# Kernel optimization log

Hardware: AMD Instinct MI355X
Metric: run time of the kernel (lower is better)

## Reference

```python
import jax, jax.numpy as jnp
import numpy as np

B, N, D_IN, D_OUT, H = 4, 2048, 1024, 1024, 16
HEAD_DIM = D_OUT // H


def setup_inputs() -> dict:
    key = jax.random.key(0)
    k1, k2, k3 = jax.random.split(key, 3)
    x = jax.random.normal(k1, (B, N, D_IN), dtype=jnp.float32)
    # torch Linear: y = x @ W.T + b; we store W already transposed as [in, out]
    w_attn = jax.random.normal(k2, (D_IN, 3 * D_OUT), dtype=jnp.float32) * (1.0 / np.sqrt(D_IN))
    w_proj = jax.random.normal(k3, (D_OUT, D_OUT), dtype=jnp.float32) * (1.0 / np.sqrt(D_OUT))
    b_proj = jnp.zeros((D_OUT,), dtype=jnp.float32)
    return {"x": x, "w_attn": w_attn, "w_proj": w_proj, "b_proj": b_proj}


def reference(x, w_attn, w_proj, b_proj):
    b, n, _ = x.shape
    qkv = x @ w_attn  # [b, n, 3*d_out]
    q, k, v = jnp.split(qkv, 3, axis=2)
    # [b, n, d_out] -> [b, h, n, head_dim]
    def to_heads(t):
        return t.reshape(b, n, H, HEAD_DIM).transpose(0, 2, 1, 3)
    q, k, v = to_heads(q), to_heads(k), to_heads(v)
    scale = 1.0 / np.sqrt(HEAD_DIM).astype(np.float32)
    att = jnp.einsum('bhqd,bhkd->bhqk', q, k) * scale  # [b, h, n, n]
    causal = jnp.tril(jnp.ones((n, n), dtype=bool))  # True = keep
    att = jnp.where(causal, att, -jnp.inf)
    att = jax.nn.softmax(att, axis=-1)
    # dropout p=0.0 -> identity
    out = jnp.einsum('bhqk,bhkd->bhqd', att, v)  # [b, h, n, head_dim]
    out = out.transpose(0, 2, 1, 3).reshape(b, n, D_OUT)
    return out @ w_proj + b_proj
```

## Files before the change

### kernel.cpp

```cpp
#include <hip/hip_runtime.h>
#include <hip/hip_bf16.h>
#include <stdint.h>

typedef short short8 __attribute__((ext_vector_type(8)));
typedef float f32x4 __attribute__((ext_vector_type(4)));

#define BQ 4
#define NSEQ 2048
#define DMODEL 1024
#define NHEAD 16
#define HDIM 64
#define MTOT 8192
#define QKV_LD 3072

#if __has_builtin(__builtin_amdgcn_exp2f)
#define EXP2(x) __builtin_amdgcn_exp2f(x)
#else
#define EXP2(x) exp2f(x)
#endif
#define C_SCL 0.18033688f

__device__ __forceinline__ uint16_t f2bf(float f) {
  uint32_t u = __builtin_bit_cast(uint32_t, f);
  uint32_t r = (u + 0x7FFFu + ((u >> 16) & 1u)) >> 16;
  return (uint16_t)r;
}
__device__ __forceinline__ float bf2f(uint16_t h) {
  uint32_t u = ((uint32_t)h) << 16;
  return __builtin_bit_cast(float, u);
}

__global__ void cast_f32_bf16_k(const float* __restrict__ in, uint16_t* __restrict__ out, int n) {
  int idx = (blockIdx.x * blockDim.x + threadIdx.x) * 4;
  int stride = gridDim.x * blockDim.x * 4;
  for (int i = idx; i < n; i += stride) {
    float4 v = *reinterpret_cast<const float4*>(in + i);
    ushort4 o;
    o.x = f2bf(v.x); o.y = f2bf(v.y); o.z = f2bf(v.z); o.w = f2bf(v.w);
    *reinterpret_cast<ushort4*>(out + i) = o;
  }
}

__global__ void transpose_cast_k(const float* __restrict__ in, uint16_t* __restrict__ out, int K, int N) {
  __shared__ float tile[32][33];
  int n0 = blockIdx.x * 32;
  int k0 = blockIdx.y * 32;
  int tx = threadIdx.x & 31;
  int ty = threadIdx.x >> 5;
#pragma unroll
  for (int r = 0; r < 4; ++r)
    tile[ty + r * 8][tx] = in[(size_t)(k0 + ty + r * 8) * N + n0 + tx];
  __syncthreads();
#pragma unroll
  for (int r = 0; r < 4; ++r)
    out[(size_t)(n0 + ty + r * 8) * K + k0 + tx] = f2bf(tile[tx][ty + r * 8]);
}

template <bool BF16_OUT>
__global__ void __launch_bounds__(256, 2)
gemm_bt_k(const uint16_t* __restrict__ A, const uint16_t* __restrict__ BT,
          void* __restrict__ Cout, const float* __restrict__ bias,
          int M, int N, int K) {
  __shared__ uint16_t As[128 * 32];
  __shared__ uint16_t Bs[128 * 32];
  const int tid = threadIdx.x;
  const int lane = tid & 63;
  const int wave = tid >> 6;
  const int wr = wave >> 1, wc = wave & 1;
  const int brow = blockIdx.y * 128;
  const int bcol = blockIdx.x * 128;
  const int l16 = lane & 15;
  const int lq = lane >> 4;

  f32x4 acc[4][4];
  const f32x4 fzero = {0.f, 0.f, 0.f, 0.f};
#pragma unroll
  for (int i = 0; i < 4; ++i)
#pragma unroll
    for (int j = 0; j < 4; ++j) acc[i][j] = fzero;

  const int ca = tid, cb = tid + 256;
  const size_t ga0 = (size_t)(brow + (ca >> 2)) * K + (ca & 3) * 8;
  const size_t ga1 = (size_t)(brow + (cb >> 2)) * K + (cb & 3) * 8;
  const size_t gb0 = (size_t)(bcol + (ca >> 2)) * K + (ca & 3) * 8;
  const size_t gb1 = (size_t)(bcol + (cb >> 2)) * K + (cb & 3) * 8;

  for (int kt = 0; kt < K; kt += 32) {
    __builtin_amdgcn_global_load_lds(
        (const __attribute__((address_space(1))) void*)(A + ga0 + kt),
        (__attribute__((address_space(3))) void*)&As[ca * 8], 16, 0, 0);
    __builtin_amdgcn_global_load_lds(
        (const __attribute__((address_space(1))) void*)(A + ga1 + kt),
        (__attribute__((address_space(3))) void*)&As[cb * 8], 16, 0, 0);
    __builtin_amdgcn_global_load_lds(
        (const __attribute__((address_space(1))) void*)(BT + gb0 + kt),
        (__attribute__((address_space(3))) void*)&Bs[ca * 8], 16, 0, 0);
    __builtin_amdgcn_global_load_lds(
        (const __attribute__((address_space(1))) void*)(BT + gb1 + kt),
        (__attribute__((address_space(3))) void*)&Bs[cb * 8], 16, 0, 0);
    __syncthreads();
    short8 af[4], bfr[4];
#pragma unroll
    for (int r = 0; r < 4; ++r) {
      af[r]  = *reinterpret_cast<const short8*>(&As[(wr * 64 + r * 16 + l16) * 32 + lq * 8]);
      bfr[r] = *reinterpret_cast<const short8*>(&Bs[(wc * 64 + r * 16 + l16) * 32 + lq * 8]);
    }
#pragma unroll
    for (int r = 0; r < 4; ++r)
#pragma unroll
      for (int c = 0; c < 4; ++c)
        acc[r][c] = __builtin_amdgcn_mfma_f32_16x16x32_bf16(af[r], bfr[c], acc[r][c], 0, 0, 0);
    __syncthreads();
  }

#pragma unroll
  for (int r = 0; r < 4; ++r) {
    const int row0 = brow + wr * 64 + r * 16 + lq * 4;
#pragma unroll
    for (int c = 0; c < 4; ++c) {
      const int col = bcol + wc * 64 + c * 16 + l16;
#pragma unroll
      for (int i = 0; i < 4; ++i) {
        if constexpr (BF16_OUT)
          reinterpret_cast<uint16_t*>(Cout)[(size_t)(row0 + i) * N + col] = f2bf(acc[r][c][i]);
        else
          reinterpret_cast<float*>(Cout)[(size_t)(row0 + i) * N + col] = acc[r][c][i] + bias[col];
      }
    }
  }
}


#define SOFTMAX_PV(SV, M_I, L_I, ACC, DIAG)                                     \
  {                                                                             \
    float tmax_ = -3e38f;                                                       \
    _Pragma("unroll") for (int nc = 0; nc < 4; ++nc) {                          \
      _Pragma("unroll") for (int i = 0; i < 4; ++i) {                           \
        float v_ = SV[nc][i];                                                   \
        if ((DIAG) && (nc * 16 + lq * 4 + i) > (w * 16 + l16)) v_ = -3e38f;     \
        SV[nc][i] = v_;                                                         \
        tmax_ = fmaxf(tmax_, v_);                                               \
      }                                                                         \
    }                                                                           \
    tmax_ = fmaxf(tmax_, __shfl_xor(tmax_, 16, 64));                            \
    tmax_ = fmaxf(tmax_, __shfl_xor(tmax_, 32, 64));                            \
    const float mn_ = fmaxf(M_I, tmax_);                                        \
    const float alpha_ = EXP2((M_I - mn_) * C_SCL);                             \
    M_I = mn_;                                                                  \
    const float mc_ = mn_ * C_SCL;                                              \
    float rsum_ = 0.f;                                                          \
    _Pragma("unroll") for (int nc = 0; nc < 4; ++nc) {                          \
      ushort4 pw_;                                                              \
      _Pragma("unroll") for (int i = 0; i < 4; ++i) {                           \
        float pv_ = EXP2(__builtin_fmaf(SV[nc][i], C_SCL, -mc_));               \
        uint16_t ph_ = f2bf(pv_);                                               \
        reinterpret_cast<uint16_t*>(&pw_)[i] = ph_;                             \
        rsum_ += bf2f(ph_);                                                     \
      }                                                                         \
      *reinterpret_cast<ushort4*>(&Ps[w][l16 * 72 + nc * 16 + lq * 4]) = pw_;   \
    }                                                                           \
    rsum_ += __shfl_xor(rsum_, 16, 64);                                         \
    rsum_ += __shfl_xor(rsum_, 32, 64);                                         \
    L_I = L_I * alpha_ + rsum_;                                                 \
    float ab_[4];                                                               \
    _Pragma("unroll") for (int i = 0; i < 4; ++i)                               \
      ab_[i] = __shfl(alpha_, lq * 4 + i, 64);                                  \
    _Pragma("unroll") for (int d4 = 0; d4 < 4; ++d4)                            \
      _Pragma("unroll") for (int i = 0; i < 4; ++i)                             \
        ACC[d4][i] *= ab_[i];                                                   \
    short8 pa0_ = *reinterpret_cast<const short8*>(&Ps[w][l16 * 72 + lq * 8]);  \
    short8 pa1_ = *reinterpret_cast<const short8*>(&Ps[w][l16 * 72 + 32 + lq * 8]); \
    _Pragma("unroll") for (int d4 = 0; d4 < 4; ++d4) {                          \
      const int drow_ = d4 * 16 + l16;                                          \
      const int xr_ = (drow_ >> 3) & 7;                                         \
      short8 vb0_ = *reinterpret_cast<const short8*>(&Vt[drow_ * 72 + ((lq ^ xr_) * 8)]); \
      short8 vb1_ = *reinterpret_cast<const short8*>(&Vt[drow_ * 72 + (((4 + lq) ^ xr_) * 8)]); \
      ACC[d4] = __builtin_amdgcn_mfma_f32_16x16x32_bf16(pa0_, vb0_, ACC[d4], 0, 0, 0); \
      ACC[d4] = __builtin_amdgcn_mfma_f32_16x16x32_bf16(pa1_, vb1_, ACC[d4], 0, 0, 0); \
    }                                                                           \
  }

__global__ void __launch_bounds__(256, 4)
attn_fwd_k(const uint16_t* __restrict__ qkv, uint16_t* __restrict__ outb) {
  const int bid = blockIdx.x;
  const int p = bid & 15;
  const int h = (bid >> 4) & 15;
  const int b = bid >> 8;
  const int qtA = p;
  const int qtB = 31 - p;
  const int tid = threadIdx.x;
  const int lane = tid & 63;
  const int w = tid >> 6;
  const int l16 = lane & 15;
  const int lq = lane >> 4;

  __shared__ uint16_t Ks[64 * 72];
  __shared__ uint16_t Vt[64 * 72];
  __shared__ uint16_t Ps[4][16 * 72];

  short8 qaA0, qaA1, qaB0, qaB1;
  {
    const size_t baseA = ((size_t)(b * NSEQ + qtA * 64 + w * 16 + l16)) * QKV_LD + h * 64 + lq * 8;
    const size_t baseB = ((size_t)(b * NSEQ + qtB * 64 + w * 16 + l16)) * QKV_LD + h * 64 + lq * 8;
    qaA0 = *reinterpret_cast<const short8*>(qkv + baseA);
    qaA1 = *reinterpret_cast<const short8*>(qkv + baseA + 32);
    qaB0 = *reinterpret_cast<const short8*>(qkv + baseB);
    qaB1 = *reinterpret_cast<const short8*>(qkv + baseB + 32);
  }

  float mA = -1e30f, lA = 0.f, mB = -1e30f, lB = 0.f;
  f32x4 accA[4], accB[4];
  const f32x4 fzero = {0.f, 0.f, 0.f, 0.f};
#pragma unroll
  for (int i = 0; i < 4; ++i) { accA[i] = fzero; accB[i] = fzero; }

  const int c0 = tid, c1 = tid + 256;
  const int r0 = c0 >> 3, d0 = (c0 & 7) * 8;
  const int r1 = c1 >> 3, d1 = (c1 & 7) * 8;
  const int ka0 = r0 * 72 + d0;
  const int ka1 = r1 * 72 + d1;
  const int vt0 = (((r0 >> 3) ^ ((d0 >> 3) & 7)) * 8) + (r0 & 7);
  const int vt1 = (((r1 >> 3) ^ ((d1 >> 3) & 7)) * 8) + (r1 & 7);

  const int ntiles = qtB + 1;
  short8 rk0, rk1, rv0, rv1;
  {
    const size_t g0 = ((size_t)(b * NSEQ + r0)) * QKV_LD + 1024 + h * 64 + d0;
    const size_t g1 = ((size_t)(b * NSEQ + r1)) * QKV_LD + 1024 + h * 64 + d1;
    rk0 = *reinterpret_cast<const short8*>(qkv + g0);
    rv0 = *reinterpret_cast<const short8*>(qkv + g0 + 1024);
    rk1 = *reinterpret_cast<const short8*>(qkv + g1);
    rv1 = *reinterpret_cast<const short8*>(qkv + g1 + 1024);
  }

  for (int jt = 0; jt < ntiles; ++jt) {
    *reinterpret_cast<short8*>(&Ks[ka0]) = rk0;
    *reinterpret_cast<short8*>(&Ks[ka1]) = rk1;
#pragma unroll
    for (int j = 0; j < 8; ++j) Vt[(d0 + j) * 72 + vt0] = (uint16_t)rv0[j];
#pragma unroll
    for (int j = 0; j < 8; ++j) Vt[(d1 + j) * 72 + vt1] = (uint16_t)rv1[j];
    if (jt + 1 < ntiles) {
      const size_t g0 = ((size_t)(b * NSEQ + (jt + 1) * 64 + r0)) * QKV_LD + 1024 + h * 64 + d0;
      const size_t g1 = ((size_t)(b * NSEQ + (jt + 1) * 64 + r1)) * QKV_LD + 1024 + h * 64 + d1;
      rk0 = *reinterpret_cast<const short8*>(qkv + g0);
      rv0 = *reinterpret_cast<const short8*>(qkv + g0 + 1024);
      rk1 = *reinterpret_cast<const short8*>(qkv + g1);
      rv1 = *reinterpret_cast<const short8*>(qkv + g1 + 1024);
    }
    __syncthreads();

    {
      f32x4 sv[4];
#pragma unroll
      for (int nc = 0; nc < 4; ++nc) {
        short8 kb0 = *reinterpret_cast<const short8*>(&Ks[(nc * 16 + l16) * 72 + lq * 8]);
        short8 kb1 = *reinterpret_cast<const short8*>(&Ks[(nc * 16 + l16) * 72 + 32 + lq * 8]);
        f32x4 s = fzero;
        s = __builtin_amdgcn_mfma_f32_16x16x32_bf16(kb0, qaB0, s, 0, 0, 0);
        s = __builtin_amdgcn_mfma_f32_16x16x32_bf16(kb1, qaB1, s, 0, 0, 0);
        sv[nc] = s;
      }
      SOFTMAX_PV(sv, mB, lB, accB, jt == qtB);
    }

    if (jt <= qtA) {
      f32x4 sv[4];
#pragma unroll
      for (int nc = 0; nc < 4; ++nc) {
        short8 kb0 = *reinterpret_cast<const short8*>(&Ks[(nc * 16 + l16) * 72 + lq * 8]);
        short8 kb1 = *reinterpret_cast<const short8*>(&Ks[(nc * 16 + l16) * 72 + 32 + lq * 8]);
        f32x4 s = fzero;
        s = __builtin_amdgcn_mfma_f32_16x16x32_bf16(kb0, qaA0, s, 0, 0, 0);
        s = __builtin_amdgcn_mfma_f32_16x16x32_bf16(kb1, qaA1, s, 0, 0, 0);
        sv[nc] = s;
      }
      SOFTMAX_PV(sv, mA, lA, accA, jt == qtA);
    }

    __syncthreads();
  }

  {
    float lb4[4];
#pragma unroll
    for (int i = 0; i < 4; ++i) lb4[i] = __shfl(lA, lq * 4 + i, 64);
    const size_t orow = (size_t)(b * NSEQ) + qtA * 64 + w * 16 + lq * 4;
#pragma unroll
    for (int d4 = 0; d4 < 4; ++d4)
#pragma unroll
      for (int i = 0; i < 4; ++i)
        outb[(orow + i) * (size_t)DMODEL + h * 64 + d4 * 16 + l16] = f2bf(accA[d4][i] / lb4[i]);
  }
  {
    float lb4[4];
#pragma unroll
    for (int i = 0; i < 4; ++i) lb4[i] = __shfl(lB, lq * 4 + i, 64);
    const size_t orow = (size_t)(b * NSEQ) + qtB * 64 + w * 16 + lq * 4;
#pragma unroll
    for (int d4 = 0; d4 < 4; ++d4)
#pragma unroll
      for (int i = 0; i < 4; ++i)
        outb[(orow + i) * (size_t)DMODEL + h * 64 + d4 * 16 + l16] = f2bf(accB[d4][i] / lb4[i]);
  }
}

extern "C" void kernel_launch(void* const* d_in, const int* in_sizes, int n_in,
                              void* d_out, int out_size, void* d_ws, size_t ws_size,
                              hipStream_t stream) {
  const float* x      = (const float*)d_in[0];
  const float* w_attn = (const float*)d_in[1];
  const float* w_proj = (const float*)d_in[2];
  const float* b_proj = (const float*)d_in[3];

  uint16_t* xb    = (uint16_t*)d_ws;
  uint16_t* wat   = xb   + (size_t)MTOT * DMODEL;
  uint16_t* wpt   = wat  + (size_t)3072 * 1024;
  uint16_t* qkvb  = wpt  + (size_t)1024 * 1024;
  uint16_t* attnb = qkvb + (size_t)MTOT * QKV_LD;

  cast_f32_bf16_k<<<2048, 256, 0, stream>>>(x, xb, MTOT * DMODEL);
  transpose_cast_k<<<dim3(3072 / 32, 1024 / 32), 256, 0, stream>>>(w_attn, wat, 1024, 3072);
  transpose_cast_k<<<dim3(1024 / 32, 1024 / 32), 256, 0, stream>>>(w_proj, wpt, 1024, 1024);

  gemm_bt_k<true><<<dim3(3072 / 128, MTOT / 128), 256, 0, stream>>>(
      xb, wat, qkvb, nullptr, MTOT, 3072, 1024);

  attn_fwd_k<<<BQ * NHEAD * 16, 256, 0, stream>>>(qkvb, attnb);

  gemm_bt_k<false><<<dim3(1024 / 128, MTOT / 128), 256, 0, stream>>>(
      attnb, wpt, d_out, b_proj, MTOT, 1024, 1024);
}
```

Measured before the change: 203.0 us.

## Keep softmax probabilities in registers by permuting the V tile layout

Removes the per-wave shared-memory round trip for the P tile in the attention kernel. The bf16 probabilities are packed straight into the MFMA A-operand registers, and the V transpose into shared memory is re-permuted so the key ordering matches the register layout of P. This drops one LDS store and two LDS loads per softmax step and frees the Ps buffer, which may raise occupancy. The cost is more complex index math for the V scatter, and correctness depends on the permutation matching exactly.

```diff
diff --git a/kernel.cpp b/kernel.cpp
--- a/kernel.cpp
+++ b/kernel.cpp
@@ -130,6 +130,59 @@
   }
 }
 
+__global__ void __launch_bounds__(256, 4)
+attn_fwd_k(const uint16_t* __restrict__ qkv, uint16_t* __restrict__ outb) {
+  const int bid = blockIdx.x;
+  const int p = bid & 15;
+  const int h = (bid >> 4) & 15;
+  const int b = bid >> 8;
+  const int qtA = p;
+  const int qtB = 31 - p;
+  const int tid = threadIdx.x;
+  const int lane = tid & 63;
+  const int w = tid >> 6;
+  const int l16 = lane & 15;
+  const int lq = lane >> 4;
+
+  __shared__ uint16_t Ks[64 * 72];
+  __shared__ uint16_t Vt[64 * 72];
+
+  short8 qaA0, qaA1, qaB0, qaB1;
+  {
+    const size_t baseA = ((size_t)(b * NSEQ + qtA * 64 + w * 16 + l16)) * QKV_LD + h * 64 + lq * 8;
+    const size_t baseB = ((size_t)(b * NSEQ + qtB * 64 + w * 16 + l16)) * QKV_LD + h * 64 + lq * 8;
+    qaA0 = *reinterpret_cast<const short8*>(qkv + baseA);
+    qaA1 = *reinterpret_cast<const short8*>(qkv + baseA + 32);
+    qaB0 = *reinterpret_cast<const short8*>(qkv + baseB);
+    qaB1 = *reinterpret_cast<const short8*>(qkv + baseB + 32);
+  }
+
+  float mA = -1e30f, lA = 0.f, mB = -1e30f, lB = 0.f;
+  f32x4 accA[4], accB[4];
+  const f32x4 fzero = {0.f, 0.f, 0.f, 0.f};
+#pragma unroll
+  for (int i = 0; i < 4; ++i) { accA[i] = fzero; accB[i] = fzero; }
+
+  const int r0 = tid >> 3, d0 = (tid & 7) * 8;
+  const int ka0 = r0 * 72 + d0;
+  const int ka1 = (r0 + 32) * 72 + d0;
+  const int lqt = (r0 >> 2) & 3;
+  const int nc0 = r0 >> 4;
+  const int m0 = d0 >> 3;
+  const int jo = (nc0 & 1) * 4 + (r0 & 3);
+  const int vcol0 = (((2 * lqt) ^ m0) * 8) + jo;
+  const int vcol1 = (((2 * lqt + 1) ^ m0) * 8) + jo;
+
+  const int ntiles = qtB + 1;
+  short8 rk0, rk1, rv0, rv1;
+  {
+    const size_t g0 = ((size_t)(b * NSEQ + r0)) * QKV_LD + 1024 + h * 64 + d0;
+    const size_t g1 = ((size_t)(b * NSEQ + r0 + 32)) * QKV_LD + 1024 + h * 64 + d0;
+    rk0 = *reinterpret_cast<const short8*>(qkv + g0);
+    rv0 = *reinterpret_cast<const short8*>(qkv + g0 + 1024);
+    rk1 = *reinterpret_cast<const short8*>(qkv + g1);
+    rv1 = *reinterpret_cast<const short8*>(qkv + g1 + 1024);
+  }
 
 #define SOFTMAX_PV(SV, M_I, L_I, ACC, DIAG)                                     \
   {                                                                             \
@@ -149,15 +202,15 @@
     M_I = mn_;                                                                  \
     const float mc_ = mn_ * C_SCL;                                              \
     float rsum_ = 0.f;                                                          \
+    short8 pa0_, pa1_;                                                          \
     _Pragma("unroll") for (int nc = 0; nc < 4; ++nc) {                          \
-      ushort4 pw_;                                                              \
       _Pragma("unroll") for (int i = 0; i < 4; ++i) {                           \
         float pv_ = EXP2(__builtin_fmaf(SV[nc][i], C_SCL, -mc_));               \
         uint16_t ph_ = f2bf(pv_);                                               \
-        reinterpret_cast<uint16_t*>(&pw_)[i] = ph_;                             \
+        if (nc < 2) pa0_[nc * 4 + i] = (short)ph_;                              \
+        else        pa1_[(nc - 2) * 4 + i] = (short)ph_;                        \
         rsum_ += bf2f(ph_);                                                     \
       }                                                                         \
-      *reinterpret_cast<ushort4*>(&Ps[w][l16 * 72 + nc * 16 + lq * 4]) = pw_;   \
     }                                                                           \
     rsum_ += __shfl_xor(rsum_, 16, 64);                                         \
     rsum_ += __shfl_xor(rsum_, 32, 64);                                         \
@@ -168,81 +221,26 @@
     _Pragma("unroll") for (int d4 = 0; d4 < 4; ++d4)                            \
       _Pragma("unroll") for (int i = 0; i < 4; ++i)                             \
         ACC[d4][i] *= ab_[i];                                                   \
-    short8 pa0_ = *reinterpret_cast<const short8*>(&Ps[w][l16 * 72 + lq * 8]);  \
-    short8 pa1_ = *reinterpret_cast<const short8*>(&Ps[w][l16 * 72 + 32 + lq * 8]); \
     _Pragma("unroll") for (int d4 = 0; d4 < 4; ++d4) {                          \
       const int drow_ = d4 * 16 + l16;                                          \
       const int xr_ = (drow_ >> 3) & 7;                                         \
-      short8 vb0_ = *reinterpret_cast<const short8*>(&Vt[drow_ * 72 + ((lq ^ xr_) * 8)]); \
-      short8 vb1_ = *reinterpret_cast<const short8*>(&Vt[drow_ * 72 + (((4 + lq) ^ xr_) * 8)]); \
+      short8 vb0_ = *reinterpret_cast<const short8*>(&Vt[drow_ * 72 + (((2 * lq) ^ xr_) * 8)]); \
+      short8 vb1_ = *reinterpret_cast<const short8*>(&Vt[drow_ * 72 + (((2 * lq + 1) ^ xr_) * 8)]); \
       ACC[d4] = __builtin_amdgcn_mfma_f32_16x16x32_bf16(pa0_, vb0_, ACC[d4], 0, 0, 0); \
       ACC[d4] = __builtin_amdgcn_mfma_f32_16x16x32_bf16(pa1_, vb1_, ACC[d4], 0, 0, 0); \
     }                                                                           \
   }
 
-__global__ void __launch_bounds__(256, 4)
-attn_fwd_k(const uint16_t* __restrict__ qkv, uint16_t* __restrict__ outb) {
-  const int bid = blockIdx.x;
-  const int p = bid & 15;
-  const int h = (bid >> 4) & 15;
-  const int b = bid >> 8;
-  const int qtA = p;
-  const int qtB = 31 - p;
-  const int tid = threadIdx.x;
-  const int lane = tid & 63;
-  const int w = tid >> 6;
-  const int l16 = lane & 15;
-  const int lq = lane >> 4;
-
-  __shared__ uint16_t Ks[64 * 72];
-  __shared__ uint16_t Vt[64 * 72];
-  __shared__ uint16_t Ps[4][16 * 72];
-
-  short8 qaA0, qaA1, qaB0, qaB1;
-  {
-    const size_t baseA = ((size_t)(b * NSEQ + qtA * 64 + w * 16 + l16)) * QKV_LD + h * 64 + lq * 8;
-    const size_t baseB = ((size_t)(b * NSEQ + qtB * 64 + w * 16 + l16)) * QKV_LD + h * 64 + lq * 8;
-    qaA0 = *reinterpret_cast<const short8*>(qkv + baseA);
-    qaA1 = *reinterpret_cast<const short8*>(qkv + baseA + 32);
-    qaB0 = *reinterpret_cast<const short8*>(qkv + baseB);
-    qaB1 = *reinterpret_cast<const short8*>(qkv + baseB + 32);
-  }
-
-  float mA = -1e30f, lA = 0.f, mB = -1e30f, lB = 0.f;
-  f32x4 accA[4], accB[4];
-  const f32x4 fzero = {0.f, 0.f, 0.f, 0.f};
-#pragma unroll
-  for (int i = 0; i < 4; ++i) { accA[i] = fzero; accB[i] = fzero; }
-
-  const int c0 = tid, c1 = tid + 256;
-  const int r0 = c0 >> 3, d0 = (c0 & 7) * 8;
-  const int r1 = c1 >> 3, d1 = (c1 & 7) * 8;
-  const int ka0 = r0 * 72 + d0;
-  const int ka1 = r1 * 72 + d1;
-  const int vt0 = (((r0 >> 3) ^ ((d0 >> 3) & 7)) * 8) + (r0 & 7);
-  const int vt1 = (((r1 >> 3) ^ ((d1 >> 3) & 7)) * 8) + (r1 & 7);
-
-  const int ntiles = qtB + 1;
-  short8 rk0, rk1, rv0, rv1;
-  {
-    const size_t g0 = ((size_t)(b * NSEQ + r0)) * QKV_LD + 1024 + h * 64 + d0;
-    const size_t g1 = ((size_t)(b * NSEQ + r1)) * QKV_LD + 1024 + h * 64 + d1;
-    rk0 = *reinterpret_cast<const short8*>(qkv + g0);
-    rv0 = *reinterpret_cast<const short8*>(qkv + g0 + 1024);
-    rk1 = *reinterpret_cast<const short8*>(qkv + g1);
-    rv1 = *reinterpret_cast<const short8*>(qkv + g1 + 1024);
-  }
-
   for (int jt = 0; jt < ntiles; ++jt) {
     *reinterpret_cast<short8*>(&Ks[ka0]) = rk0;
     *reinterpret_cast<short8*>(&Ks[ka1]) = rk1;
 #pragma unroll
-    for (int j = 0; j < 8; ++j) Vt[(d0 + j) * 72 + vt0] = (uint16_t)rv0[j];
-#pragma unroll
-    for (int j = 0; j < 8; ++j) Vt[(d1 + j) * 72 + vt1] = (uint16_t)rv1[j];
+    for (int j = 0; j < 8; ++j) Vt[(d0 + j) * 72 + vcol0] = (uint16_t)rv0[j];
+#pragma unroll
+    for (int j = 0; j < 8; ++j) Vt[(d0 + j) * 72 + vcol1] = (uint16_t)rv1[j];
     if (jt + 1 < ntiles) {
       const size_t g0 = ((size_t)(b * NSEQ + (jt + 1) * 64 + r0)) * QKV_LD + 1024 + h * 64 + d0;
-      const size_t g1 = ((size_t)(b * NSEQ + (jt + 1) * 64 + r1)) * QKV_LD + 1024 + h * 64 + d1;
+      const size_t g1 = ((size_t)(b * NSEQ + (jt + 1) * 64 + r0 + 32)) * QKV_LD + 1024 + h * 64 + d0;
       rk0 = *reinterpret_cast<const short8*>(qkv + g0);
       rv0 = *reinterpret_cast<const short8*>(qkv + g0 + 1024);
       rk1 = *reinterpret_cast<const short8*>(qkv + g1);
```

Measured after the change: 282.2 us. 39.0% more time.
